# Performance work log

Hardware: AMD Instinct MI355X
Metric: run time of the kernel (lower is better)

Reference implementation:

```python
import jax, jax.numpy as jnp
import numpy as np
import math

EMBED_DIM = 1024
NUM_HEADS = 16
HEAD_DIM = EMBED_DIM // NUM_HEADS
INPUT_DIM = 1024


def setup_inputs() -> dict:
    key = jax.random.key(0)
    k_x, k_wqkv, k_wout = jax.random.split(key, 3)
    x = jax.random.normal(k_x, (4, 1, 2048, INPUT_DIM), dtype=jnp.float32)
    # xavier_uniform bounds
    def xavier(k, shape):
        fan_out, fan_in = shape
        bound = math.sqrt(6.0 / (fan_in + fan_out))
        return jax.random.uniform(k, shape, jnp.float32, -bound, bound)
    w_qkv = xavier(k_wqkv, (3 * EMBED_DIM, INPUT_DIM))
    b_qkv = jnp.zeros((3 * EMBED_DIM,), jnp.float32)
    w_out = xavier(k_wout, (EMBED_DIM, EMBED_DIM))
    b_out = jnp.zeros((EMBED_DIM,), jnp.float32)
    return {"x": x, "w_qkv": w_qkv, "b_qkv": b_qkv, "w_out": w_out, "b_out": b_out}


def reference(x, w_qkv, b_qkv, w_out, b_out):
    B, y, S, _ = x.shape  # y must be 1 (module reshape constraint)
    # QKV projection: [B, y, S, 3E]
    qkv = jnp.einsum('bysd,ed->byse', x, w_qkv) + b_qkv
    # reshape to [B, S, H, 3*head_dim] then [B, H, S, 3*head_dim]
    qkv = qkv.reshape(B, S, NUM_HEADS, 3 * HEAD_DIM).transpose(0, 2, 1, 3)
    q, k, v = jnp.split(qkv, 3, axis=-1)  # each [B, H, S, head_dim]
    logits = jnp.einsum('bhqd,bhkd->bhqk', q, k) / math.sqrt(HEAD_DIM)
    attn = jax.nn.softmax(logits, axis=-1)  # [B, H, S, S]
    vals = jnp.einsum('bhqk,bhkd->bhqd', attn, v)
    vals = vals.transpose(0, 2, 1, 3).reshape(B, S, EMBED_DIM)
    return jnp.einsum('bse,oe->bso', vals, w_out) + b_out  # [B, S, E]
```

## Files before the change

### kernel.cpp

```cpp
#include <hip/hip_runtime.h>

typedef __bf16 bf16;
typedef __bf16 bf16x8 __attribute__((ext_vector_type(8)));
typedef __bf16 bf16x4 __attribute__((ext_vector_type(4)));
typedef float f32x4 __attribute__((ext_vector_type(4)));
typedef float f32x16 __attribute__((ext_vector_type(16)));
typedef unsigned int u32x4 __attribute__((ext_vector_type(4)));

#define SM_SCALE 0.18033688011f

__device__ __forceinline__ f32x4 mfma16(bf16x8 a, bf16x8 b, f32x4 c) {
    return __builtin_amdgcn_mfma_f32_16x16x32_bf16(a, b, c, 0, 0, 0);
}
__device__ __forceinline__ f32x16 mfma32(bf16x8 a, bf16x8 b, f32x16 c) {
    return __builtin_amdgcn_mfma_f32_32x32x16_bf16(a, b, c, 0, 0, 0);
}

__device__ __forceinline__ void gload_lds16(const void* g, void* l) {
    __builtin_amdgcn_global_load_lds((const __attribute__((address_space(1))) void*)g,
                                     (__attribute__((address_space(3))) void*)l,
                                     16, 0, 0);
}

__device__ __forceinline__ unsigned cvtpk_bf16(float lo, float hi) {
    unsigned r;
    asm("v_cvt_pk_bf16_f32 %0, %1, %2" : "=v"(r) : "v"(lo), "v"(hi));
    return r;
}
__device__ __forceinline__ void plane32_swap(unsigned& a, unsigned& b) {
    asm("v_permlane32_swap_b32 %0, %1" : "+v"(a), "+v"(b));
}
__device__ __forceinline__ float vexp2(float x) {
    float r;
    asm("v_exp_f32 %0, %1" : "=v"(r) : "v"(x));
    return r;
}
__device__ __forceinline__ float vrcp(float x) {
    float r;
    asm("v_rcp_f32 %0, %1" : "=v"(r) : "v"(x));
    return r;
}

__device__ __forceinline__ void vpack_store(char* VwB, unsigned vwlow, bf16x8 v0, bf16x8 v1) {
    const u32x4 a = __builtin_bit_cast(u32x4, v0);
    const u32x4 b = __builtin_bit_cast(u32x4, v1);
#pragma unroll
    for (int j = 0; j < 8; ++j) {
        const unsigned sel = (j & 1) ? 0x07060302u : 0x05040100u;
        const unsigned w = __builtin_amdgcn_perm(b[j >> 1], a[j >> 1], sel);
        *(unsigned*)(VwB + j * 128 + (vwlow ^ (unsigned)(j << 4))) = w;
    }
}

__global__ void cvt_all(const float* __restrict__ x, const float* __restrict__ wq,
                        const float* __restrict__ wo, bf16* __restrict__ xb,
                        bf16* __restrict__ wqb, bf16* __restrict__ wob) {
    constexpr int NX = (8192 * 1024) / 4, NQ = (3072 * 1024) / 4, NO = (1024 * 1024) / 4;
    const int stride = gridDim.x * blockDim.x;
    for (int i = blockIdx.x * blockDim.x + threadIdx.x; i < NX + NQ + NO; i += stride) {
        const float* src;
        bf16* dst;
        int li;
        if (i < NX)           { src = x;  dst = xb;  li = i; }
        else if (i < NX + NQ) { src = wq; dst = wqb; li = i - NX; }
        else                  { src = wo; dst = wob; li = i - NX - NQ; }
        const f32x4 v = ((const f32x4*)src)[li];
        bf16x4 o;
#pragma unroll
        for (int j = 0; j < 4; ++j) o[j] = (bf16)v[j];
        ((bf16x4*)dst)[li] = o;
    }
}

template <typename OutT, bool QSCALE>
__global__ __launch_bounds__(256) void gemm_bt(const bf16* __restrict__ A,
                                               const bf16* __restrict__ Bw,
                                               const float* __restrict__ bias,
                                               OutT* __restrict__ C,
                                               int M, int N, int K) {
    constexpr int BM = 128, BN = 128, BK = 64;
    __shared__ bf16 As[BM * BK];
    __shared__ bf16 Bs[BN * BK];
    const int tid = threadIdx.x;
    const int wave = tid >> 6, lane = tid & 63;
    const int ln15 = lane & 15, g4 = lane >> 4;
    const int m0 = blockIdx.x * BM, n0 = blockIdx.y * BN;
    const int wm = (wave >> 1) * 64, wn = (wave & 1) * 64;
    f32x4 acc[4][4] = {};
    const int nk = K / BK;
    for (int kt = 0; kt < nk; ++kt) {
        const int kb = kt * BK;
#pragma unroll
        for (int c = 0; c < 4; ++c) {
            const int chunk = c * 4 + wave;
            const int lin = chunk * 1024 + lane * 16;
            const int r = lin >> 7;
            const int ce = (lin & 127) >> 1;
            gload_lds16(A + (size_t)(m0 + r) * K + kb + ce, (char*)As + chunk * 1024);
            gload_lds16(Bw + (size_t)(n0 + r) * K + kb + ce, (char*)Bs + chunk * 1024);
        }
        __syncthreads();
#pragma unroll
        for (int kc = 0; kc < 2; ++kc) {
            bf16x8 a[4], b[4];
#pragma unroll
            for (int mi = 0; mi < 4; ++mi)
                a[mi] = *(const bf16x8*)&As[(wm + mi * 16 + ln15) * BK + kc * 32 + g4 * 8];
#pragma unroll
            for (int nj = 0; nj < 4; ++nj)
                b[nj] = *(const bf16x8*)&Bs[(wn + nj * 16 + ln15) * BK + kc * 32 + g4 * 8];
#pragma unroll
            for (int mi = 0; mi < 4; ++mi)
#pragma unroll
                for (int nj = 0; nj < 4; ++nj)
                    acc[mi][nj] = mfma16(a[mi], b[nj], acc[mi][nj]);
        }
        __syncthreads();
    }
    float bv[4], sc[4];
#pragma unroll
    for (int nj = 0; nj < 4; ++nj) {
        const int col = n0 + wn + nj * 16 + ln15;
        bv[nj] = bias[col];
        sc[nj] = (QSCALE && (col % 192) < 64) ? SM_SCALE : 1.0f;
    }
#pragma unroll
    for (int mi = 0; mi < 4; ++mi) {
#pragma unroll
        for (int nj = 0; nj < 4; ++nj) {
            const int col = n0 + wn + nj * 16 + ln15;
#pragma unroll
            for (int i = 0; i < 4; ++i) {
                const int row = m0 + wm + mi * 16 + g4 * 4 + i;
                C[(size_t)row * N + col] = (OutT)((acc[mi][nj][i] + bv[nj]) * sc[nj]);
            }
        }
    }
}

#define ATTN_ITER(CUR, PRE)                                                          \
  {                                                                                  \
    if (PRE) {                                                                       \
      gload_lds16(kp, (char*)Ks + ((CUR ^ 1) * 8192) + wave * 1024);                 \
      gload_lds16(kp + 32 * 3072, (char*)Ks + ((CUR ^ 1) * 8192) + (4 + wave) * 1024); \
      v0 = *(const bf16x8*)vp;                                                       \
      v1 = *(const bf16x8*)(vp + 3072);                                              \
      kp += 64 * 3072;                                                               \
      vp += 64 * 3072;                                                               \
    }                                                                                \
    _Pragma("unroll") for (int kh = 0; kh < 2; ++kh) {                               \
      f32x16 s;                                                                      \
      __builtin_amdgcn_s_setprio(1);                                                 \
      s = mfma32(*(const bf16x8*)(kra[0] + CUR * 8192 + kh * 4096), qf[0], z16);     \
      _Pragma("unroll") for (int dc = 1; dc < 4; ++dc) {                             \
        const bf16x8 kf = *(const bf16x8*)(kra[dc] + CUR * 8192 + kh * 4096);        \
        s = mfma32(kf, qf[dc], s);                                                   \
      }                                                                              \
      __builtin_amdgcn_s_setprio(0);                                                 \
      unsigned pk[8];                                                                \
      _Pragma("unroll") for (int m = 0; m < 8; ++m)                                  \
        pk[m] = cvtpk_bf16(vexp2(s[2 * m]), vexp2(s[2 * m + 1]));                    \
      plane32_swap(pk[0], pk[2]);                                                    \
      plane32_swap(pk[1], pk[3]);                                                    \
      plane32_swap(pk[4], pk[6]);                                                    \
      plane32_swap(pk[5], pk[7]);                                                    \
      const bf16x8 pf0 = __builtin_bit_cast(bf16x8, (u32x4){pk[0], pk[1], pk[2], pk[3]}); \
      const bf16x8 pf1 = __builtin_bit_cast(bf16x8, (u32x4){pk[4], pk[5], pk[6], pk[7]}); \
      __builtin_amdgcn_s_setprio(1);                                                 \
      {                                                                              \
        const bf16x8 va0 = *(const bf16x8*)(VsB + CUR * 8192 + (vroff0 ^ (kh * 64)));       \
        const bf16x8 vc0 = *(const bf16x8*)(VsB + CUR * 8192 + (vroff0 ^ (kh * 64 + 32)));  \
        o0 = mfma32(pf0, va0, o0);                                                   \
        o0 = mfma32(pf1, vc0, o0);                                                   \
        const bf16x8 va1 = *(const bf16x8*)(VsB + CUR * 8192 + (vroff1 ^ (kh * 64)));       \
        const bf16x8 vc1 = *(const bf16x8*)(VsB + CUR * 8192 + (vroff1 ^ (kh * 64 + 32)));  \
        o1 = mfma32(pf0, va1, o1);                                                   \
        o1 = mfma32(pf1, vc1, o1);                                                   \
        dsumC = mfma32(pf0, ones, dsumC);                                            \
        dsumC = mfma32(pf1, ones, dsumC);                                            \
      }                                                                              \
      __builtin_amdgcn_s_setprio(0);                                                 \
    }                                                                                \
    if (PRE) vpack_store((char*)Ks + 16384 + ((CUR ^ 1) * 8192) + vd8 * 128, vwlow, v0, v1); \
    __syncthreads();                                                                 \
  }

__global__ __launch_bounds__(256) void attn_fa(const bf16* __restrict__ qkv,
                                               bf16* __restrict__ vals) {
    const int b = blockIdx.x >> 4, h = blockIdx.x & 15;
    const int q0 = blockIdx.y * 128;
    const int tid = threadIdx.x, wave = tid >> 6, lane = tid & 63;
    const int ln31 = lane & 31, hi = lane >> 5;

    __shared__ bf16 Ks[2 * 4096 + 2 * 4096];

    const size_t base = ((size_t)b * 2048) * 3072 + (size_t)h * 192;
    const bf16* Qb = qkv + base;

    bf16x8 qf[4];
    {
        const size_t qr = (size_t)(q0 + wave * 32 + ln31) * 3072;
#pragma unroll
        for (int dc = 0; dc < 4; ++dc)
            qf[dc] = *(const bf16x8*)(Qb + qr + dc * 16 + hi * 8);
    }

    const int krow0 = wave * 8 + (lane >> 3);
    const int kgsw = ((lane & 7) ^ (lane >> 3)) * 8;
    const bf16* kp = qkv + base + 64 + (size_t)krow0 * 3072 + kgsw;
    const int vr2 = tid & 31, vd8 = (tid >> 5) * 8;
    const bf16* vp = qkv + base + 128 + (size_t)(2 * vr2) * 3072 + vd8;
    const unsigned vwlow = 4u * (unsigned)vr2;

    const int kxor = (ln31 & 7) << 4;
    const char* kra[4];
#pragma unroll
    for (int dc = 0; dc < 4; ++dc)
        kra[dc] = (char*)Ks + ln31 * 128 + ((dc * 32 + hi * 16) ^ kxor);
    const char* const VsB = (char*)Ks + 16384;
    const unsigned vroff0 = (unsigned)(ln31 * 128 + ((hi * 16) ^ kxor));
    const unsigned vroff1 = vroff0 + 32 * 128;

    const bf16x8 ones = __builtin_bit_cast(bf16x8, (u32x4){0x3F803F80u, 0x3F803F80u,
                                                           0x3F803F80u, 0x3F803F80u});
    const f32x16 z16 = {};
    f32x16 o0 = {}, o1 = {}, dsumC = {};
    bf16x8 v0, v1;

    gload_lds16(kp, (char*)Ks + wave * 1024);
    gload_lds16(kp + 32 * 3072, (char*)Ks + (4 + wave) * 1024);
    v0 = *(const bf16x8*)vp;
    v1 = *(const bf16x8*)(vp + 3072);
    kp += 64 * 3072;
    vp += 64 * 3072;
    vpack_store((char*)Ks + 16384 + vd8 * 128, vwlow, v0, v1);
    __syncthreads();

    for (int tp = 0; tp < 15; ++tp) {
        ATTN_ITER(0, true)
        ATTN_ITER(1, true)
    }
    ATTN_ITER(0, true)
    ATTN_ITER(1, false)

#pragma unroll
    for (int r = 0; r < 16; ++r) {
        const float invq = vrcp(dsumC[r]);
        const int qloc = (r & 3) + 8 * (r >> 2) + 4 * hi;
        const size_t orow = ((size_t)b * 2048 + q0 + wave * 32 + qloc) * 1024 + h * 64;
        vals[orow + ln31]      = (bf16)(o0[r] * invq);
        vals[orow + 32 + ln31] = (bf16)(o1[r] * invq);
    }
}

extern "C" void kernel_launch(void* const* d_in, const int* in_sizes, int n_in,
                              void* d_out, int out_size, void* d_ws, size_t ws_size,
                              hipStream_t stream) {
    const float* x     = (const float*)d_in[0];
    const float* w_qkv = (const float*)d_in[1];
    const float* b_qkv = (const float*)d_in[2];
    const float* w_out = (const float*)d_in[3];
    const float* b_out = (const float*)d_in[4];
    float* out = (float*)d_out;

    char* ws = (char*)d_ws;
    bf16* xb   = (bf16*)ws;
    bf16* wqb  = (bf16*)(ws + (16u << 20));
    bf16* wob  = (bf16*)(ws + (22u << 20));
    bf16* qkvb = (bf16*)(ws + (24u << 20));
    bf16* valb = xb;

    cvt_all<<<dim3(2048), dim3(256), 0, stream>>>(x, w_qkv, w_out, xb, wqb, wob);

    gemm_bt<bf16, true><<<dim3(64, 24), dim3(256), 0, stream>>>(xb, wqb, b_qkv, qkvb,
                                                                8192, 3072, 1024);
    attn_fa<<<dim3(64, 16), dim3(256), 0, stream>>>(qkvb, valb);
    gemm_bt<float, false><<<dim3(64, 8), dim3(256), 0, stream>>>(valb, wob, b_out, out,
                                                                 8192, 1024, 1024);
}
```

Before: 210.5 us.

## Replace GEMM main loop with 4-stage async LDS pipeline and swizzled layout

```diff
diff --git a/kernel.cpp b/kernel.cpp
--- a/kernel.cpp
+++ b/kernel.cpp
@@ -72,55 +72,86 @@
     }
 }
 
+#define G_TILE(BUF, VM, DOSTAGE)                                            \
+  {                                                                         \
+    asm volatile("s_waitcnt vmcnt(" #VM ")" ::: "memory");                  \
+    __builtin_amdgcn_s_barrier();                                           \
+    bf16x8 af[4], bfr[4];                                                   \
+    _Pragma("unroll") for (int mf = 0; mf < 4; ++mf)                        \
+      af[mf] = *(const bf16x8*)(baseA[BUF] + mf * 1024);                    \
+    _Pragma("unroll") for (int nf = 0; nf < 4; ++nf)                        \
+      bfr[nf] = *(const bf16x8*)(baseB[BUF] + nf * 1024);                   \
+    if (DOSTAGE) {                                                          \
+      gload_lds16(apA0, ldA + (((BUF) + 3) & 3) * 16384);                   \
+      gload_lds16(apA1, ldA + (((BUF) + 3) & 3) * 16384 + 4096);            \
+      gload_lds16(apB0, ldB + (((BUF) + 3) & 3) * 16384);                   \
+      gload_lds16(apB1, ldB + (((BUF) + 3) & 3) * 16384 + 4096);            \
+      apA0 += 32; apA1 += 32; apB0 += 32; apB1 += 32;                       \
+    }                                                                       \
+    __builtin_amdgcn_s_setprio(1);                                          \
+    _Pragma("unroll") for (int mf = 0; mf < 4; ++mf)                        \
+      _Pragma("unroll") for (int nf = 0; nf < 4; ++nf)                      \
+        acc[mf][nf] = mfma16(af[mf], bfr[nf], acc[mf][nf]);                 \
+    __builtin_amdgcn_s_setprio(0);                                          \
+  }
+
 template <typename OutT, bool QSCALE>
-__global__ __launch_bounds__(256) void gemm_bt(const bf16* __restrict__ A,
-                                               const bf16* __restrict__ Bw,
-                                               const float* __restrict__ bias,
-                                               OutT* __restrict__ C,
-                                               int M, int N, int K) {
-    constexpr int BM = 128, BN = 128, BK = 64;
-    __shared__ bf16 As[BM * BK];
-    __shared__ bf16 Bs[BN * BK];
+__global__ __launch_bounds__(256) void gemm4d(const bf16* __restrict__ A,
+                                              const bf16* __restrict__ Bw,
+                                              const float* __restrict__ bias,
+                                              OutT* __restrict__ C,
+                                              int M, int N, int K) {
+    __shared__ char lds[4 * 16384];
     const int tid = threadIdx.x;
     const int wave = tid >> 6, lane = tid & 63;
     const int ln15 = lane & 15, g4 = lane >> 4;
-    const int m0 = blockIdx.x * BM, n0 = blockIdx.y * BN;
-    const int wm = (wave >> 1) * 64, wn = (wave & 1) * 64;
+    const int wr = wave >> 1, wc = wave & 1;
+    const int m0 = blockIdx.x * 128, n0 = blockIdx.y * 128;
+
+    const int srow = lane >> 2;
+    const int sgsw = ((lane & 3) ^ ((lane >> 2) & 3)) * 8;
+    const bf16* apA0 = A  + (size_t)(m0 + wave * 16 + srow) * K + sgsw;
+    const bf16* apA1 = A  + (size_t)(m0 + 64 + wave * 16 + srow) * K + sgsw;
+    const bf16* apB0 = Bw + (size_t)(n0 + wave * 16 + srow) * K + sgsw;
+    const bf16* apB1 = Bw + (size_t)(n0 + 64 + wave * 16 + srow) * K + sgsw;
+    char* const ldA = (char*)lds + wave * 1024;
+    char* const ldB = (char*)lds + 8192 + wave * 1024;
+
+    const int kxr = (g4 * 16) ^ ((ln15 & 3) << 4);
+    const char* baseA[4];
+    const char* baseB[4];
+#pragma unroll
+    for (int b = 0; b < 4; ++b) {
+        baseA[b] = (const char*)lds + b * 16384 + (wr * 64 + ln15) * 64 + kxr;
+        baseB[b] = (const char*)lds + b * 16384 + 8192 + (wc * 64 + ln15) * 64 + kxr;
+    }
+
     f32x4 acc[4][4] = {};
-    const int nk = K / BK;
-    for (int kt = 0; kt < nk; ++kt) {
-        const int kb = kt * BK;
-#pragma unroll
-        for (int c = 0; c < 4; ++c) {
-            const int chunk = c * 4 + wave;
-            const int lin = chunk * 1024 + lane * 16;
-            const int r = lin >> 7;
-            const int ce = (lin & 127) >> 1;
-            gload_lds16(A + (size_t)(m0 + r) * K + kb + ce, (char*)As + chunk * 1024);
-            gload_lds16(Bw + (size_t)(n0 + r) * K + kb + ce, (char*)Bs + chunk * 1024);
-        }
-        __syncthreads();
-#pragma unroll
-        for (int kc = 0; kc < 2; ++kc) {
-            bf16x8 a[4], b[4];
-#pragma unroll
-            for (int mi = 0; mi < 4; ++mi)
-                a[mi] = *(const bf16x8*)&As[(wm + mi * 16 + ln15) * BK + kc * 32 + g4 * 8];
-#pragma unroll
-            for (int nj = 0; nj < 4; ++nj)
-                b[nj] = *(const bf16x8*)&Bs[(wn + nj * 16 + ln15) * BK + kc * 32 + g4 * 8];
-#pragma unroll
-            for (int mi = 0; mi < 4; ++mi)
-#pragma unroll
-                for (int nj = 0; nj < 4; ++nj)
-                    acc[mi][nj] = mfma16(a[mi], b[nj], acc[mi][nj]);
-        }
-        __syncthreads();
-    }
+
+#pragma unroll
+    for (int p = 0; p < 3; ++p) {
+        gload_lds16(apA0, ldA + p * 16384);
+        gload_lds16(apA1, ldA + p * 16384 + 4096);
+        gload_lds16(apB0, ldB + p * 16384);
+        gload_lds16(apB1, ldB + p * 16384 + 4096);
+        apA0 += 32; apA1 += 32; apB0 += 32; apB1 += 32;
+    }
+
+    for (int g = 0; g < 7; ++g) {
+        G_TILE(0, 8, 1)
+        G_TILE(1, 8, 1)
+        G_TILE(2, 8, 1)
+        G_TILE(3, 8, 1)
+    }
+    G_TILE(0, 8, 1)
+    G_TILE(1, 8, 0)
+    G_TILE(2, 4, 0)
+    G_TILE(3, 0, 0)
+
     float bv[4], sc[4];
 #pragma unroll
     for (int nj = 0; nj < 4; ++nj) {
-        const int col = n0 + wn + nj * 16 + ln15;
+        const int col = n0 + wc * 64 + nj * 16 + ln15;
         bv[nj] = bias[col];
         sc[nj] = (QSCALE && (col % 192) < 64) ? SM_SCALE : 1.0f;
     }
@@ -128,10 +159,10 @@
     for (int mi = 0; mi < 4; ++mi) {
 #pragma unroll
         for (int nj = 0; nj < 4; ++nj) {
-            const int col = n0 + wn + nj * 16 + ln15;
+            const int col = n0 + wc * 64 + nj * 16 + ln15;
 #pragma unroll
             for (int i = 0; i < 4; ++i) {
-                const int row = m0 + wm + mi * 16 + g4 * 4 + i;
+                const int row = m0 + wr * 64 + mi * 16 + g4 * 4 + i;
                 C[(size_t)row * N + col] = (OutT)((acc[mi][nj][i] + bv[nj]) * sc[nj]);
             }
         }
@@ -272,9 +303,9 @@
 
     cvt_all<<<dim3(2048), dim3(256), 0, stream>>>(x, w_qkv, w_out, xb, wqb, wob);
 
-    gemm_bt<bf16, true><<<dim3(64, 24), dim3(256), 0, stream>>>(xb, wqb, b_qkv, qkvb,
-                                                                8192, 3072, 1024);
+    gemm4d<bf16, true><<<dim3(64, 24), dim3(256), 0, stream>>>(xb, wqb, b_qkv, qkvb,
+                                                               8192, 3072, 1024);
     attn_fa<<<dim3(64, 16), dim3(256), 0, stream>>>(qkvb, valb);
-    gemm_bt<float, false><<<dim3(64, 8), dim3(256), 0, stream>>>(valb, wob, b_out, out,
-                                                                 8192, 1024, 1024);
-}
+    gemm4d<float, false><<<dim3(64, 8), dim3(256), 0, stream>>>(valb, wob, b_out, out,
+                                                                8192, 1024, 1024);
+}
```

Result: faster. 192.1 us (-8.8%).
